# Optimization experiments

Measured on AMD Instinct MI355X. Metric: run time of the kernel, lower is better.

The kernel has to match this reference:

```python
import jax, jax.numpy as jnp
import numpy as np

N_HEAD, DIM, D_K, D_V = 16, 1024, 64, 64
B, L = 4, 2048


def setup_inputs() -> dict:
    key = jax.random.key(0)
    ks = jax.random.split(key, 8)
    def xavier(k, shape, fan_in, fan_out):
        std = float(np.sqrt(2.0 / (fan_in + fan_out)))
        return jax.random.normal(k, shape, dtype=jnp.float32) * std
    return {
        "q": jax.random.normal(ks[0], (B, L, DIM), dtype=jnp.float32),
        "k": jax.random.normal(ks[1], (B, L, DIM), dtype=jnp.float32),
        "v": jax.random.normal(ks[2], (B, L, DIM), dtype=jnp.float32),
        "w_q": xavier(ks[3], (N_HEAD, DIM, D_K), DIM, D_K),
        "w_k": xavier(ks[4], (N_HEAD, DIM, D_K), DIM, D_K),
        "w_v": xavier(ks[5], (N_HEAD, DIM, D_V), DIM, D_V),
        "proj_w": xavier(ks[6], (DIM, N_HEAD * D_V), N_HEAD * D_V, DIM),
        "proj_b": jnp.zeros((DIM,), dtype=jnp.float32),
    }


def reference(q, k, v, w_q, w_k, w_v, proj_w, proj_b):
    batch, len_q, dim = q.shape
    # NOTE: original scales by sqrt(dim) (model dim), not sqrt(d_k)
    scale = jnp.asarray(np.sqrt(dim), dtype=q.dtype)
    # per-head projections: [h, b, q, dk]
    qh = jnp.einsum('bqd,hdk->hbqk', q, w_q)
    kh = jnp.einsum('bsd,hdk->hbsk', k, w_k)
    vh = jnp.einsum('bsd,hdv->hbsv', v, w_v)
    scores = jnp.einsum('hbqk,hbsk->hbqs', qh, kh) / scale
    attn = jax.nn.softmax(scores, axis=-1)
    out = jnp.einsum('hbqs,hbsv->hbqv', attn, vh)
    # concat heads along last dim: [b, q, h*dv] (head-major order, matching torch.cat(split))
    out = jnp.transpose(out, (1, 2, 0, 3)).reshape(batch, len_q, -1)
    # output projection (dropout is identity at eval)
    return out @ proj_w.T + proj_b
```

## Files before the change

kernel.cpp:

```cpp
#include <hip/hip_runtime.h>
#include <hip/hip_bf16.h>
#include <stdint.h>

#define NH 16
#define DM 1024
#define DKV 64
#define BB 4
#define LL 2048
#define MT (BB*LL)
#define NT (LL/64)

typedef __bf16 bf16;
typedef __bf16 bf16x8 __attribute__((ext_vector_type(8)));
typedef float f32x4 __attribute__((ext_vector_type(4)));
typedef float f32x16 __attribute__((ext_vector_type(16)));
typedef unsigned int u32x2 __attribute__((ext_vector_type(2)));
typedef unsigned int u32x4 __attribute__((ext_vector_type(4)));

__device__ __forceinline__ void gload_lds16(const void* g, void* l) {
  __builtin_amdgcn_global_load_lds(
      (const __attribute__((address_space(1))) unsigned int*)g,
      (__attribute__((address_space(3))) unsigned int*)l, 16, 0, 0);
}

__device__ __forceinline__ unsigned short bfbits(float x) {
  bf16 b = (bf16)x;
  return __builtin_bit_cast(unsigned short, b);
}

__device__ __forceinline__ float fast_exp2(float x) {
#if defined(__has_builtin)
#if __has_builtin(__builtin_amdgcn_exp2f)
  return __builtin_amdgcn_exp2f(x);
#else
  float r; asm("v_exp_f32 %0, %1" : "=v"(r) : "v"(x)); return r;
#endif
#else
  float r; asm("v_exp_f32 %0, %1" : "=v"(r) : "v"(x)); return r;
#endif
}

#if defined(__has_builtin)
#if __has_builtin(__builtin_amdgcn_permlane32_swap)
#define HAVE_PLSWAP 1
#endif
#endif

__device__ __forceinline__ u32x2 plswap(unsigned int a, unsigned int b, int hi) {
#ifdef HAVE_PLSWAP
  auto rr = __builtin_amdgcn_permlane32_swap(a, b, false, false);
  u32x2 r; r.x = rr[0]; r.y = rr[1];
  return r;
#else
  unsigned int pa = (unsigned int)__shfl_xor((int)a, 32);
  unsigned int pb_ = (unsigned int)__shfl_xor((int)b, 32);
  u32x2 r;
  r.x = hi ? pb_ : a;
  r.y = hi ? b : pa;
  return r;
#endif
}

__global__ __launch_bounds__(256) void cast3_f32_to_bf16(const float* __restrict__ i0,
                                                         const float* __restrict__ i1,
                                                         const float* __restrict__ i2,
                                                         bf16* __restrict__ o0,
                                                         bf16* __restrict__ o1,
                                                         bf16* __restrict__ o2, int n8) {
  const float* in = blockIdx.y == 0 ? i0 : (blockIdx.y == 1 ? i1 : i2);
  bf16* out = blockIdx.y == 0 ? o0 : (blockIdx.y == 1 ? o1 : o2);
  int i = blockIdx.x * blockDim.x + threadIdx.x;
  if (i >= n8) return;
  const float4* p = (const float4*)in + (size_t)i * 2;
  float4 a = p[0], b = p[1];
  bf16x8 r;
  r[0] = (bf16)a.x; r[1] = (bf16)a.y; r[2] = (bf16)a.z; r[3] = (bf16)a.w;
  r[4] = (bf16)b.x; r[5] = (bf16)b.y; r[6] = (bf16)b.z; r[7] = (bf16)b.w;
  *((bf16x8*)out + i) = r;
}

__global__ __launch_bounds__(256) void cast_f32_to_bf16(const float* __restrict__ in,
                                                        bf16* __restrict__ out, int n8) {
  int i = blockIdx.x * blockDim.x + threadIdx.x;
  if (i >= n8) return;
  const float4* p = (const float4*)in + (size_t)i * 2;
  float4 a = p[0], b = p[1];
  bf16x8 r;
  r[0] = (bf16)a.x; r[1] = (bf16)a.y; r[2] = (bf16)a.z; r[3] = (bf16)a.w;
  r[4] = (bf16)b.x; r[5] = (bf16)b.y; r[6] = (bf16)b.z; r[7] = (bf16)b.w;
  *((bf16x8*)out + i) = r;
}

__global__ __launch_bounds__(256) void repack_w(const float* __restrict__ w0, const float* __restrict__ w1,
                                                const float* __restrict__ w2,
                                                bf16* __restrict__ o0, bf16* __restrict__ o1,
                                                bf16* __restrict__ o2) {
  const float* w = blockIdx.z == 0 ? w0 : (blockIdx.z == 1 ? w1 : w2);
  bf16* o = blockIdx.z == 0 ? o0 : (blockIdx.z == 1 ? o1 : o2);
  __shared__ float t[64][65];
  int h = blockIdx.y, d0 = blockIdx.x * 64;
  const float* src = w + ((size_t)h * DM + d0) * DKV;
  for (int i = threadIdx.x; i < 64 * 64; i += 256) {
    int r = i >> 6, c = i & 63;
    t[r][c] = src[(size_t)r * DKV + c];
  }
  __syncthreads();
  for (int i = threadIdx.x; i < 64 * 64; i += 256) {
    int kk = i >> 6, d = i & 63;
    o[((size_t)(h * 64 + kk)) * DM + d0 + d] = (bf16)t[d][kk];
  }
}

__global__ __launch_bounds__(256) void gemm_qkv(const bf16* __restrict__ Xq, const bf16* __restrict__ Xk,
                                                const bf16* __restrict__ Xv, const bf16* __restrict__ Wqt,
                                                const bf16* __restrict__ Wkt, const bf16* __restrict__ Wvt,
                                                bf16* __restrict__ QH, bf16* __restrict__ KH,
                                                bf16* __restrict__ VT) {
  __shared__ bf16 sA[128 * 64];
  __shared__ bf16 sB[128 * 64];
  const int mode = blockIdx.z;
  const bf16* A  = mode == 0 ? Xq : (mode == 1 ? Xk : Xv);
  const bf16* Bt = mode == 0 ? Wqt : (mode == 1 ? Wkt : Wvt);
  const int tid = threadIdx.x;
  const int w = tid >> 6, l = tid & 63;
  const int c = l & 15, g4 = l >> 4;
  const int wm = w >> 1, wn = w & 1;
  const int m0 = blockIdx.y * 128, n0 = blockIdx.x * 128;

  f32x4 acc[4][4] = {};
  for (int kt = 0; kt < 1024; kt += 64) {
#pragma unroll
    for (int i = 0; i < 4; ++i) {
      int blk = i * 4 + w;
      int row = blk * 8 + (l >> 3);
      int g = (l & 7) ^ (row & 7);
      gload_lds16(A + ((size_t)(m0 + row)) * 1024 + kt + g * 8, (char*)sA + blk * 1024);
      gload_lds16(Bt + ((size_t)(n0 + row)) * 1024 + kt + g * 8, (char*)sB + blk * 1024);
    }
    __syncthreads();
#pragma unroll
    for (int ks = 0; ks < 2; ++ks) {
      bf16x8 af[4], bfr[4];
#pragma unroll
      for (int x = 0; x < 4; ++x) {
        int ar = wm * 64 + x * 16 + c;
        af[x] = *(const bf16x8*)((const char*)sA + ar * 128 + (((ks * 4 + g4) ^ (ar & 7)) * 16));
        int br = wn * 64 + x * 16 + c;
        bfr[x] = *(const bf16x8*)((const char*)sB + br * 128 + (((ks * 4 + g4) ^ (br & 7)) * 16));
      }
#pragma unroll
      for (int x = 0; x < 4; ++x)
#pragma unroll
        for (int y = 0; y < 4; ++y)
          acc[x][y] = __builtin_amdgcn_mfma_f32_16x16x32_bf16(af[x], bfr[y], acc[x][y], 0, 0, 0);
    }
    __syncthreads();
  }

  const int mm = m0 + wm * 64, nn = n0 + wn * 64;
  if (mode < 2) {
    bf16* O = mode == 0 ? QH : KH;
    const float s = (mode == 0) ? 0.03125f * 1.44269504088896f : 1.0f;
#pragma unroll
    for (int x = 0; x < 4; ++x)
#pragma unroll
      for (int y = 0; y < 4; ++y)
#pragma unroll
        for (int r = 0; r < 4; ++r) {
          int m = mm + x * 16 + g4 * 4 + r;
          int n = nn + y * 16 + c;
          O[(size_t)m * 1024 + n] = (bf16)(acc[x][y][r] * s);
        }
  } else {
    bf16* O = VT;
#pragma unroll
    for (int x = 0; x < 4; ++x)
#pragma unroll
      for (int y = 0; y < 4; ++y) {
        int mb = mm + x * 16 + g4 * 4;
        int n = nn + y * 16 + c;
        int bb2 = mb >> 11, sidx = mb & 2047;
        int hh2 = n >> 6, dv = n & 63;
        unsigned int u0 = bfbits(acc[x][y][0]) | ((unsigned int)bfbits(acc[x][y][1]) << 16);
        unsigned int u1 = bfbits(acc[x][y][2]) | ((unsigned int)bfbits(acc[x][y][3]) << 16);
        *(uint2*)(O + ((size_t)((hh2 * 4 + bb2) * 64 + dv)) * LL + sidx) = make_uint2(u0, u1);
      }
  }
}

__global__ __launch_bounds__(256) void gemm_proj(const bf16* __restrict__ A, const bf16* __restrict__ Bt,
                                                 float* __restrict__ Out, const float* __restrict__ bias) {
  __shared__ bf16 sA[128 * 64];
  __shared__ bf16 sB[128 * 64];
  const int tid = threadIdx.x;
  const int w = tid >> 6, l = tid & 63;
  const int c = l & 15, g4 = l >> 4;
  const int wm = w >> 1, wn = w & 1;
  const int m0 = blockIdx.y * 128, n0 = blockIdx.x * 128;

  f32x4 acc[4][4] = {};
  for (int kt = 0; kt < 1024; kt += 64) {
#pragma unroll
    for (int i = 0; i < 4; ++i) {
      int blk = i * 4 + w;
      int row = blk * 8 + (l >> 3);
      int g = (l & 7) ^ (row & 7);
      gload_lds16(A + ((size_t)(m0 + row)) * 1024 + kt + g * 8, (char*)sA + blk * 1024);
      gload_lds16(Bt + ((size_t)(n0 + row)) * 1024 + kt + g * 8, (char*)sB + blk * 1024);
    }
    __syncthreads();
#pragma unroll
    for (int ks = 0; ks < 2; ++ks) {
      bf16x8 af[4], bfr[4];
#pragma unroll
      for (int x = 0; x < 4; ++x) {
        int ar = wm * 64 + x * 16 + c;
        af[x] = *(const bf16x8*)((const char*)sA + ar * 128 + (((ks * 4 + g4) ^ (ar & 7)) * 16));
        int br = wn * 64 + x * 16 + c;
        bfr[x] = *(const bf16x8*)((const char*)sB + br * 128 + (((ks * 4 + g4) ^ (br & 7)) * 16));
      }
#pragma unroll
      for (int x = 0; x < 4; ++x)
#pragma unroll
        for (int y = 0; y < 4; ++y)
          acc[x][y] = __builtin_amdgcn_mfma_f32_16x16x32_bf16(af[x], bfr[y], acc[x][y], 0, 0, 0);
    }
    __syncthreads();
  }

  const int mm = m0 + wm * 64, nn = n0 + wn * 64;
#pragma unroll
  for (int x = 0; x < 4; ++x)
#pragma unroll
    for (int y = 0; y < 4; ++y)
#pragma unroll
      for (int r = 0; r < 4; ++r) {
        int m = mm + x * 16 + g4 * 4 + r;
        int n = nn + y * 16 + c;
        Out[(size_t)m * 1024 + n] = acc[x][y][r] + bias[n];
      }
}

__global__ __launch_bounds__(256, 2) void attn_kernel(const bf16* __restrict__ qh,
                                                      const bf16* __restrict__ kh,
                                                      const bf16* __restrict__ vt,
                                                      bf16* __restrict__ o) {
  __shared__ bf16 sK[4][64 * 64];
  __shared__ bf16 sV[4][64 * 64];
  const int tid = threadIdx.x, w = tid >> 6, l = tid & 63;
  const int c = l & 31, hi = l >> 5;
  const int bh = blockIdx.x, b = bh & 3, h = bh >> 2;
  const int q0 = blockIdx.y * 256 + w * 64;

  const bf16* qbase = qh + ((size_t)(b * LL)) * DM + h * 64;
  const bf16* kbase = kh + ((size_t)(b * LL)) * DM + h * 64;
  const bf16* vbase = vt + ((size_t)((h * 4 + b) * 64)) * LL;

  bf16x8 qfA[4], qfB[4];
#pragma unroll
  for (int ks = 0; ks < 4; ++ks) {
    qfA[ks] = *(const bf16x8*)(qbase + (size_t)(q0 + c) * DM + ks * 16 + hi * 8);
    qfB[ks] = *(const bf16x8*)(qbase + (size_t)(q0 + 32 + c) * DM + ks * 16 + hi * 8);
  }

  bf16x8 onesf;
#pragma unroll
  for (int i = 0; i < 8; ++i) onesf[i] = (bf16)1.0f;

  f32x16 oA0 = {}, oA1 = {}, oB0 = {}, oB1 = {};
  f32x16 lAa = {}, lBa = {};

  auto STAGE = [&](int bufi, int kv0) {
#pragma unroll
    for (int j = 0; j < 2; ++j) {
      int gi = w * 128 + j * 64 + l;
      int row = gi >> 3;
      int g = (gi & 7) ^ (row & 7);
      gload_lds16(kbase + (size_t)(kv0 + row) * DM + g * 8,
                  (char*)sK[bufi] + (w * 128 + j * 64) * 16);
      gload_lds16(vbase + (size_t)row * LL + kv0 + g * 8,
                  (char*)sV[bufi] + (w * 128 + j * 64) * 16);
    }
  };

  auto EXPPACK = [&](f32x16& st0, f32x16& st1, bf16x8* pb) {
#pragma unroll
    for (int r = 0; r < 16; ++r) st0[r] = fast_exp2(st0[r]);
#pragma unroll
    for (int r = 0; r < 16; ++r) st1[r] = fast_exp2(st1[r]);
#pragma unroll
    for (int t = 0; t < 2; ++t) {
      const f32x16& st = t ? st1 : st0;
      unsigned int u[4][2];
#pragma unroll
      for (int g2 = 0; g2 < 4; ++g2) {
        u[g2][0] = (unsigned int)bfbits(st[4 * g2 + 0]) | ((unsigned int)bfbits(st[4 * g2 + 1]) << 16);
        u[g2][1] = (unsigned int)bfbits(st[4 * g2 + 2]) | ((unsigned int)bfbits(st[4 * g2 + 3]) << 16);
      }
      u32x2 s0 = plswap(u[0][0], u[1][0], hi);
      u32x2 s1 = plswap(u[0][1], u[1][1], hi);
      u32x4 w0; w0.x = s0.x; w0.y = s1.x; w0.z = s0.y; w0.w = s1.y;
      pb[2 * t] = __builtin_bit_cast(bf16x8, w0);
      u32x2 s2 = plswap(u[2][0], u[3][0], hi);
      u32x2 s3 = plswap(u[2][1], u[3][1], hi);
      u32x4 w1; w1.x = s2.x; w1.y = s3.x; w1.z = s2.y; w1.w = s3.y;
      pb[2 * t + 1] = __builtin_bit_cast(bf16x8, w1);
    }
  };

  auto TILE = [&](int bufi) {
    const char* Kb = (const char*)sK[bufi];
    const char* Vb = (const char*)sV[bufi];

    bf16x8 kf[8];
#pragma unroll
    for (int ks = 0; ks < 4; ++ks) {
      int slot = ((ks * 2 + hi) ^ (c & 7)) * 16;
      kf[ks]     = *(const bf16x8*)(Kb + c * 128 + slot);
      kf[4 + ks] = *(const bf16x8*)(Kb + (32 + c) * 128 + slot);
    }
    f32x16 sA0 = {}, sA1 = {}, sB0 = {}, sB1 = {};
    __builtin_amdgcn_s_setprio(1);
#pragma unroll
    for (int ks = 0; ks < 4; ++ks) {
      sA0 = __builtin_amdgcn_mfma_f32_32x32x16_bf16(kf[ks],     qfA[ks], sA0, 0, 0, 0);
      sA1 = __builtin_amdgcn_mfma_f32_32x32x16_bf16(kf[4 + ks], qfA[ks], sA1, 0, 0, 0);
    }
#pragma unroll
    for (int ks = 0; ks < 4; ++ks) {
      sB0 = __builtin_amdgcn_mfma_f32_32x32x16_bf16(kf[ks],     qfB[ks], sB0, 0, 0, 0);
      sB1 = __builtin_amdgcn_mfma_f32_32x32x16_bf16(kf[4 + ks], qfB[ks], sB1, 0, 0, 0);
    }
    __builtin_amdgcn_s_setprio(0);

    bf16x8 pbA[4];
    EXPPACK(sA0, sA1, pbA);

    bf16x8 vf[8];
#pragma unroll
    for (int ks = 0; ks < 4; ++ks) {
      int slot = ((ks * 2 + hi) ^ (c & 7)) * 16;
      vf[ks]     = *(const bf16x8*)(Vb + c * 128 + slot);
      vf[4 + ks] = *(const bf16x8*)(Vb + (32 + c) * 128 + slot);
    }
    __builtin_amdgcn_s_setprio(1);
#pragma unroll
    for (int ks = 0; ks < 4; ++ks) {
      oA0 = __builtin_amdgcn_mfma_f32_32x32x16_bf16(vf[ks],     pbA[ks], oA0, 0, 0, 0);
      oA1 = __builtin_amdgcn_mfma_f32_32x32x16_bf16(vf[4 + ks], pbA[ks], oA1, 0, 0, 0);
      lAa = __builtin_amdgcn_mfma_f32_32x32x16_bf16(onesf,      pbA[ks], lAa, 0, 0, 0);
    }
    __builtin_amdgcn_s_setprio(0);

    bf16x8 pbB[4];
    EXPPACK(sB0, sB1, pbB);
    __builtin_amdgcn_s_setprio(1);
#pragma unroll
    for (int ks = 0; ks < 4; ++ks) {
      oB0 = __builtin_amdgcn_mfma_f32_32x32x16_bf16(vf[ks],     pbB[ks], oB0, 0, 0, 0);
      oB1 = __builtin_amdgcn_mfma_f32_32x32x16_bf16(vf[4 + ks], pbB[ks], oB1, 0, 0, 0);
      lBa = __builtin_amdgcn_mfma_f32_32x32x16_bf16(onesf,      pbB[ks], lBa, 0, 0, 0);
    }
    __builtin_amdgcn_s_setprio(0);
  };

  STAGE(0, 0);
  STAGE(1, 64);

  for (int wd = 0; wd < 16; ++wd) {
    __builtin_amdgcn_s_barrier();
    int t2 = 2 * wd + 2;
    if (t2 < NT) {
      STAGE(t2 & 3, t2 * 64);
      STAGE((t2 + 1) & 3, (t2 + 1) * 64);
      asm volatile("s_waitcnt vmcnt(8)" ::: "memory");
    } else {
      asm volatile("s_waitcnt vmcnt(0)" ::: "memory");
    }
    TILE((2 * wd) & 3);
    TILE((2 * wd + 1) & 3);
  }

  bf16* ob = o + ((size_t)(b * LL)) * DM + h * 64;
  {
    float inv = 1.0f / lAa[0];
#pragma unroll
    for (int dt = 0; dt < 2; ++dt) {
      const f32x16& oc = dt ? oA1 : oA0;
#pragma unroll
      for (int rg = 0; rg < 4; ++rg) {
        int dv0 = dt * 32 + rg * 8 + hi * 4;
        unsigned int u0 = (unsigned int)bfbits(oc[rg * 4 + 0] * inv) |
                          ((unsigned int)bfbits(oc[rg * 4 + 1] * inv) << 16);
        unsigned int u1 = (unsigned int)bfbits(oc[rg * 4 + 2] * inv) |
                          ((unsigned int)bfbits(oc[rg * 4 + 3] * inv) << 16);
        *(uint2*)(ob + (size_t)(q0 + c) * DM + dv0) = make_uint2(u0, u1);
      }
    }
  }
  {
    float inv = 1.0f / lBa[0];
#pragma unroll
    for (int dt = 0; dt < 2; ++dt) {
      const f32x16& oc = dt ? oB1 : oB0;
#pragma unroll
      for (int rg = 0; rg < 4; ++rg) {
        int dv0 = dt * 32 + rg * 8 + hi * 4;
        unsigned int u0 = (unsigned int)bfbits(oc[rg * 4 + 0] * inv) |
                          ((unsigned int)bfbits(oc[rg * 4 + 1] * inv) << 16);
        unsigned int u1 = (unsigned int)bfbits(oc[rg * 4 + 2] * inv) |
                          ((unsigned int)bfbits(oc[rg * 4 + 3] * inv) << 16);
        *(uint2*)(ob + (size_t)(q0 + 32 + c) * DM + dv0) = make_uint2(u0, u1);
      }
    }
  }
}

extern "C" void kernel_launch(void* const* d_in, const int* in_sizes, int n_in,
                              void* d_out, int out_size, void* d_ws, size_t ws_size,
                              hipStream_t stream) {
  const float* q  = (const float*)d_in[0];
  const float* k  = (const float*)d_in[1];
  const float* v  = (const float*)d_in[2];
  const float* wq = (const float*)d_in[3];
  const float* wk = (const float*)d_in[4];
  const float* wv = (const float*)d_in[5];
  const float* pw = (const float*)d_in[6];
  const float* pb = (const float*)d_in[7];
  float* out = (float*)d_out;

  char* ws = (char*)d_ws;
  const size_t SX = (size_t)MT * DM * 2;
  const size_t SW = (size_t)DM * DM * 2;
  bf16* Xq  = (bf16*)(ws);
  bf16* Xk  = (bf16*)(ws + SX);
  bf16* Xv  = (bf16*)(ws + 2 * SX);
  bf16* Wqt = (bf16*)(ws + 3 * SX);
  bf16* Wkt = (bf16*)(ws + 3 * SX + SW);
  bf16* Wvt = (bf16*)(ws + 3 * SX + 2 * SW);
  bf16* Wp  = (bf16*)(ws + 3 * SX + 3 * SW);
  bf16* QH  = (bf16*)(ws + 3 * SX + 4 * SW);
  bf16* KH  = (bf16*)(ws + 4 * SX + 4 * SW);
  bf16* VT  = (bf16*)(ws + 5 * SX + 4 * SW);
  bf16* OO  = Xq;

  const int nx8 = MT * DM / 8;
  cast3_f32_to_bf16<<<dim3(nx8 / 256, 3), 256, 0, stream>>>(q, k, v, Xq, Xk, Xv, nx8);
  const int nw8 = DM * DM / 8;
  cast_f32_to_bf16<<<dim3(nw8 / 256), 256, 0, stream>>>(pw, Wp, nw8);
  repack_w<<<dim3(16, 16, 3), 256, 0, stream>>>(wq, wk, wv, Wqt, Wkt, Wvt);

  gemm_qkv<<<dim3(8, 64, 3), 256, 0, stream>>>(Xq, Xk, Xv, Wqt, Wkt, Wvt, QH, KH, VT);

  attn_kernel<<<dim3(64, 8), 256, 0, stream>>>(QH, KH, VT, OO);

  gemm_proj<<<dim3(8, 64), 256, 0, stream>>>(OO, Wp, out, pb);
}
```

Measured before the change: 219.2 us.

## Rewrite QKV GEMM as 256x256 tile, double-buffered, 8-wave pipelined kernel

Replaces the 128x128 single-buffered QKV projection GEMM with a 256x256 tile kernel using 512 threads and double-buffered LDS. Global-to-LDS loads for the next K tile are issued in halves between MFMA phases, with explicit vmcnt gating, barriers and setprio. The aim is to hide load latency behind compute and raise arithmetic intensity per block. It uses 128 KB of LDS per block, which limits occupancy, and produces fewer blocks (384), which risks wave-quantization imbalance across CUs.

```diff
diff --git a/kernel.cpp b/kernel.cpp
--- a/kernel.cpp
+++ b/kernel.cpp
@@ -16,6 +16,8 @@
 typedef float f32x16 __attribute__((ext_vector_type(16)));
 typedef unsigned int u32x2 __attribute__((ext_vector_type(2)));
 typedef unsigned int u32x4 __attribute__((ext_vector_type(4)));
+
+template <int V> struct ic { static constexpr int v = V; };
 
 __device__ __forceinline__ void gload_lds16(const void* g, void* l) {
   __builtin_amdgcn_global_load_lds(
@@ -111,74 +113,123 @@
   }
 }
 
-__global__ __launch_bounds__(256) void gemm_qkv(const bf16* __restrict__ Xq, const bf16* __restrict__ Xk,
-                                                const bf16* __restrict__ Xv, const bf16* __restrict__ Wqt,
-                                                const bf16* __restrict__ Wkt, const bf16* __restrict__ Wvt,
-                                                bf16* __restrict__ QH, bf16* __restrict__ KH,
-                                                bf16* __restrict__ VT) {
-  __shared__ bf16 sA[128 * 64];
-  __shared__ bf16 sB[128 * 64];
+__global__ __launch_bounds__(512, 2) void gemm_qkv256(const bf16* __restrict__ Xq, const bf16* __restrict__ Xk,
+                                                      const bf16* __restrict__ Xv, const bf16* __restrict__ Wqt,
+                                                      const bf16* __restrict__ Wkt, const bf16* __restrict__ Wvt,
+                                                      bf16* __restrict__ QH, bf16* __restrict__ KH,
+                                                      bf16* __restrict__ VT) {
+  __shared__ bf16 sA[2][256 * 64];
+  __shared__ bf16 sB[2][256 * 64];
   const int mode = blockIdx.z;
-  const bf16* A  = mode == 0 ? Xq : (mode == 1 ? Xk : Xv);
-  const bf16* Bt = mode == 0 ? Wqt : (mode == 1 ? Wkt : Wvt);
+  const bf16* Ap  = mode == 0 ? Xq : (mode == 1 ? Xk : Xv);
+  const bf16* Btp = mode == 0 ? Wqt : (mode == 1 ? Wkt : Wvt);
   const int tid = threadIdx.x;
-  const int w = tid >> 6, l = tid & 63;
-  const int c = l & 15, g4 = l >> 4;
-  const int wm = w >> 1, wn = w & 1;
-  const int m0 = blockIdx.y * 128, n0 = blockIdx.x * 128;
-
-  f32x4 acc[4][4] = {};
-  for (int kt = 0; kt < 1024; kt += 64) {
-#pragma unroll
-    for (int i = 0; i < 4; ++i) {
-      int blk = i * 4 + w;
-      int row = blk * 8 + (l >> 3);
-      int g = (l & 7) ^ (row & 7);
-      gload_lds16(A + ((size_t)(m0 + row)) * 1024 + kt + g * 8, (char*)sA + blk * 1024);
-      gload_lds16(Bt + ((size_t)(n0 + row)) * 1024 + kt + g * 8, (char*)sB + blk * 1024);
-    }
-    __syncthreads();
-#pragma unroll
-    for (int ks = 0; ks < 2; ++ks) {
-      bf16x8 af[4], bfr[4];
-#pragma unroll
-      for (int x = 0; x < 4; ++x) {
-        int ar = wm * 64 + x * 16 + c;
-        af[x] = *(const bf16x8*)((const char*)sA + ar * 128 + (((ks * 4 + g4) ^ (ar & 7)) * 16));
-        int br = wn * 64 + x * 16 + c;
-        bfr[x] = *(const bf16x8*)((const char*)sB + br * 128 + (((ks * 4 + g4) ^ (br & 7)) * 16));
-      }
-#pragma unroll
-      for (int x = 0; x < 4; ++x)
-#pragma unroll
-        for (int y = 0; y < 4; ++y)
-          acc[x][y] = __builtin_amdgcn_mfma_f32_16x16x32_bf16(af[x], bfr[y], acc[x][y], 0, 0, 0);
-    }
-    __syncthreads();
-  }
-
-  const int mm = m0 + wm * 64, nn = n0 + wn * 64;
+  const int wid = tid >> 6, l = tid & 63;
+  const int cc = l & 15, g4 = l >> 4;
+  const int wr = wid >> 2, wc = wid & 3;
+  const int m0 = blockIdx.y * 256, n0 = blockIdx.x * 256;
+
+  f32x4 acc[8][4] = {};
+
+  auto STAGEH = [&](auto SB_, auto SI_, auto SH_, int stile) {
+    constexpr int SBUF = decltype(SB_)::v, SISB = decltype(SI_)::v, SHALF = decltype(SH_)::v;
+    int kk = (stile < 16 ? stile : 15) * 64;
+    const bf16* sp = SISB ? Btp : Ap;
+    int b0 = SISB ? n0 : m0;
+    char* db = (char*)(SISB ? &sB[SBUF][0] : &sA[SBUF][0]);
+#pragma unroll
+    for (int j = 0; j < 2; ++j) {
+      int gb = (j * 8 + wid) * 64;
+      int g = gb + l;
+      int rl = g >> 3, gl = g & 7;
+      int row = SHALF * 128 + rl;
+      int slot = gl ^ (row & 7);
+      gload_lds16(sp + (size_t)(b0 + row) * 1024 + kk + slot * 8,
+                  db + (SHALF * 1024 + gb) * 16);
+    }
+  };
+
+  auto PHASE = [&](auto MH_, auto NH_, auto BUF_, auto SB_, auto SI_, auto SH_,
+                   int stile, auto GATE_) {
+    constexpr int MH = decltype(MH_)::v, NHF = decltype(NH_)::v, BUF = decltype(BUF_)::v;
+    constexpr int GATE = decltype(GATE_)::v;
+    bf16x8 af[4][2], bfv[2][2];
+#pragma unroll
+    for (int x2 = 0; x2 < 4; ++x2) {
+      int ar = (2 * (MH * 4 + x2) + wr) * 16 + cc;
+#pragma unroll
+      for (int ks = 0; ks < 2; ++ks)
+        af[x2][ks] = *(const bf16x8*)((const char*)&sA[BUF][0] + ar * 128 +
+                                      (((ks * 4 + g4) ^ (ar & 7)) * 16));
+    }
+#pragma unroll
+    for (int y2 = 0; y2 < 2; ++y2) {
+      int br = (4 * (NHF * 2 + y2) + wc) * 16 + cc;
+#pragma unroll
+      for (int ks = 0; ks < 2; ++ks)
+        bfv[y2][ks] = *(const bf16x8*)((const char*)&sB[BUF][0] + br * 128 +
+                                       (((ks * 4 + g4) ^ (br & 7)) * 16));
+    }
+    STAGEH(SB_, SI_, SH_, stile);
+    __builtin_amdgcn_s_barrier();
+    asm volatile("s_waitcnt lgkmcnt(0)" ::: "memory");
+    __builtin_amdgcn_sched_barrier(0);
+    __builtin_amdgcn_s_setprio(1);
+#pragma unroll
+    for (int x2 = 0; x2 < 4; ++x2)
+#pragma unroll
+      for (int y2 = 0; y2 < 2; ++y2)
+#pragma unroll
+        for (int ks = 0; ks < 2; ++ks)
+          acc[MH * 4 + x2][NHF * 2 + y2] = __builtin_amdgcn_mfma_f32_16x16x32_bf16(
+              af[x2][ks], bfv[y2][ks], acc[MH * 4 + x2][NHF * 2 + y2], 0, 0, 0);
+    __builtin_amdgcn_s_setprio(0);
+    if constexpr (GATE == 8) asm volatile("s_waitcnt vmcnt(8)" ::: "memory");
+    else if constexpr (GATE == 6) asm volatile("s_waitcnt vmcnt(6)" ::: "memory");
+    else if constexpr (GATE == 4) asm volatile("s_waitcnt vmcnt(4)" ::: "memory");
+    __builtin_amdgcn_s_barrier();
+  };
+
+  STAGEH(ic<0>{}, ic<0>{}, ic<0>{}, 0); STAGEH(ic<0>{}, ic<0>{}, ic<1>{}, 0);
+  STAGEH(ic<0>{}, ic<1>{}, ic<0>{}, 0); STAGEH(ic<0>{}, ic<1>{}, ic<1>{}, 0);
+  STAGEH(ic<1>{}, ic<0>{}, ic<0>{}, 1); STAGEH(ic<1>{}, ic<0>{}, ic<1>{}, 1);
+  STAGEH(ic<1>{}, ic<1>{}, ic<0>{}, 1); STAGEH(ic<1>{}, ic<1>{}, ic<1>{}, 1);
+  asm volatile("s_waitcnt vmcnt(0)" ::: "memory");
+  __builtin_amdgcn_s_barrier();
+
+  for (int i = 0; i < 8; ++i) {
+    int t0 = 2 * i;
+    PHASE(ic<0>{}, ic<0>{}, ic<0>{},  ic<1>{}, ic<0>{}, ic<1>{}, t0 + 1, ic<-1>{});
+    PHASE(ic<0>{}, ic<1>{}, ic<0>{},  ic<1>{}, ic<1>{}, ic<1>{}, t0 + 1, ic<-1>{});
+    PHASE(ic<1>{}, ic<0>{}, ic<0>{},  ic<0>{}, ic<0>{}, ic<0>{}, t0 + 2, ic<-1>{});
+    PHASE(ic<1>{}, ic<1>{}, ic<0>{},  ic<0>{}, ic<1>{}, ic<0>{}, t0 + 2, ic<8>{});
+    PHASE(ic<0>{}, ic<0>{}, ic<1>{},  ic<0>{}, ic<0>{}, ic<1>{}, t0 + 2, ic<6>{});
+    PHASE(ic<0>{}, ic<1>{}, ic<1>{},  ic<0>{}, ic<1>{}, ic<1>{}, t0 + 2, ic<-1>{});
+    PHASE(ic<1>{}, ic<0>{}, ic<1>{},  ic<1>{}, ic<0>{}, ic<0>{}, t0 + 3, ic<-1>{});
+    PHASE(ic<1>{}, ic<1>{}, ic<1>{},  ic<1>{}, ic<1>{}, ic<0>{}, t0 + 3, ic<4>{});
+  }
+
   if (mode < 2) {
     bf16* O = mode == 0 ? QH : KH;
     const float s = (mode == 0) ? 0.03125f * 1.44269504088896f : 1.0f;
 #pragma unroll
-    for (int x = 0; x < 4; ++x)
+    for (int x = 0; x < 8; ++x)
 #pragma unroll
       for (int y = 0; y < 4; ++y)
 #pragma unroll
         for (int r = 0; r < 4; ++r) {
-          int m = mm + x * 16 + g4 * 4 + r;
-          int n = nn + y * 16 + c;
+          int m = m0 + (2 * x + wr) * 16 + g4 * 4 + r;
+          int n = n0 + (4 * y + wc) * 16 + cc;
           O[(size_t)m * 1024 + n] = (bf16)(acc[x][y][r] * s);
         }
   } else {
     bf16* O = VT;
 #pragma unroll
-    for (int x = 0; x < 4; ++x)
+    for (int x = 0; x < 8; ++x)
 #pragma unroll
       for (int y = 0; y < 4; ++y) {
-        int mb = mm + x * 16 + g4 * 4;
-        int n = nn + y * 16 + c;
+        int mb = m0 + (2 * x + wr) * 16 + g4 * 4;
+        int n = n0 + (4 * y + wc) * 16 + cc;
         int bb2 = mb >> 11, sidx = mb & 2047;
         int hh2 = n >> 6, dv = n & 63;
         unsigned int u0 = bfbits(acc[x][y][0]) | ((unsigned int)bfbits(acc[x][y][1]) << 16);
@@ -450,7 +501,7 @@
   cast_f32_to_bf16<<<dim3(nw8 / 256), 256, 0, stream>>>(pw, Wp, nw8);
   repack_w<<<dim3(16, 16, 3), 256, 0, stream>>>(wq, wk, wv, Wqt, Wkt, Wvt);
 
-  gemm_qkv<<<dim3(8, 64, 3), 256, 0, stream>>>(Xq, Xk, Xv, Wqt, Wkt, Wvt, QH, KH, VT);
+  gemm_qkv256<<<dim3(4, 32, 3), 512, 0, stream>>>(Xq, Xk, Xv, Wqt, Wkt, Wvt, QH, KH, VT);
 
   attn_kernel<<<dim3(64, 8), 256, 0, stream>>>(QH, KH, VT, OO);
 
```

Measured after the change: 235.9 us. 1.08x slower.

## Split attention work across 8 waves with 32 queries each

Applied to the files above, without the earlier changes.

The attention block grows from 4 to 8 waves, and each wave now owns 32 query rows instead of 64. Per-wave registers roughly halve (one set of accumulators, K/V fragments loaded just in time), and the launch bounds request 4 blocks per CU for more latency hiding. Each thread stages one 16-byte chunk per K/V tile instead of two, and the waitcnt is adjusted to match. In exchange, each wave reads K/V from LDS for half the queries, doubling LDS read traffic per FLOP and lowering MFMA reuse per fragment load.

```diff
diff --git a/kernel.cpp b/kernel.cpp
--- a/kernel.cpp
+++ b/kernel.cpp
@@ -241,7 +241,7 @@
       }
 }
 
-__global__ __launch_bounds__(256, 2) void attn_kernel(const bf16* __restrict__ qh,
+__global__ __launch_bounds__(512, 4) void attn_kernel(const bf16* __restrict__ qh,
                                                       const bf16* __restrict__ kh,
                                                       const bf16* __restrict__ vt,
                                                       bf16* __restrict__ o) {
@@ -250,37 +250,31 @@
   const int tid = threadIdx.x, w = tid >> 6, l = tid & 63;
   const int c = l & 31, hi = l >> 5;
   const int bh = blockIdx.x, b = bh & 3, h = bh >> 2;
-  const int q0 = blockIdx.y * 256 + w * 64;
+  const int q0 = blockIdx.y * 256 + w * 32;
 
   const bf16* qbase = qh + ((size_t)(b * LL)) * DM + h * 64;
   const bf16* kbase = kh + ((size_t)(b * LL)) * DM + h * 64;
   const bf16* vbase = vt + ((size_t)((h * 4 + b) * 64)) * LL;
 
-  bf16x8 qfA[4], qfB[4];
-#pragma unroll
-  for (int ks = 0; ks < 4; ++ks) {
-    qfA[ks] = *(const bf16x8*)(qbase + (size_t)(q0 + c) * DM + ks * 16 + hi * 8);
-    qfB[ks] = *(const bf16x8*)(qbase + (size_t)(q0 + 32 + c) * DM + ks * 16 + hi * 8);
-  }
+  bf16x8 qf[4];
+#pragma unroll
+  for (int ks = 0; ks < 4; ++ks)
+    qf[ks] = *(const bf16x8*)(qbase + (size_t)(q0 + c) * DM + ks * 16 + hi * 8);
 
   bf16x8 onesf;
 #pragma unroll
   for (int i = 0; i < 8; ++i) onesf[i] = (bf16)1.0f;
 
-  f32x16 oA0 = {}, oA1 = {}, oB0 = {}, oB1 = {};
-  f32x16 lAa = {}, lBa = {};
+  f32x16 o0 = {}, o1 = {};
+  f32x16 la = {};
 
   auto STAGE = [&](int bufi, int kv0) {
-#pragma unroll
-    for (int j = 0; j < 2; ++j) {
-      int gi = w * 128 + j * 64 + l;
-      int row = gi >> 3;
-      int g = (gi & 7) ^ (row & 7);
-      gload_lds16(kbase + (size_t)(kv0 + row) * DM + g * 8,
-                  (char*)sK[bufi] + (w * 128 + j * 64) * 16);
-      gload_lds16(vbase + (size_t)row * LL + kv0 + g * 8,
-                  (char*)sV[bufi] + (w * 128 + j * 64) * 16);
-    }
+    int row = tid >> 3;
+    int g = (tid & 7) ^ (row & 7);
+    gload_lds16(kbase + (size_t)(kv0 + row) * DM + g * 8,
+                (char*)sK[bufi] + w * 1024);
+    gload_lds16(vbase + (size_t)row * LL + kv0 + g * 8,
+                (char*)sV[bufi] + w * 1024);
   };
 
   auto EXPPACK = [&](f32x16& st0, f32x16& st1, bf16x8* pb) {
@@ -312,54 +306,30 @@
     const char* Kb = (const char*)sK[bufi];
     const char* Vb = (const char*)sV[bufi];
 
-    bf16x8 kf[8];
+    f32x16 st0 = {}, st1 = {};
+    __builtin_amdgcn_s_setprio(1);
 #pragma unroll
     for (int ks = 0; ks < 4; ++ks) {
       int slot = ((ks * 2 + hi) ^ (c & 7)) * 16;
-      kf[ks]     = *(const bf16x8*)(Kb + c * 128 + slot);
-      kf[4 + ks] = *(const bf16x8*)(Kb + (32 + c) * 128 + slot);
-    }
-    f32x16 sA0 = {}, sA1 = {}, sB0 = {}, sB1 = {};
+      bf16x8 k0 = *(const bf16x8*)(Kb + c * 128 + slot);
+      bf16x8 k1 = *(const bf16x8*)(Kb + (32 + c) * 128 + slot);
+      st0 = __builtin_amdgcn_mfma_f32_32x32x16_bf16(k0, qf[ks], st0, 0, 0, 0);
+      st1 = __builtin_amdgcn_mfma_f32_32x32x16_bf16(k1, qf[ks], st1, 0, 0, 0);
+    }
+    __builtin_amdgcn_s_setprio(0);
+
+    bf16x8 pb[4];
+    EXPPACK(st0, st1, pb);
+
     __builtin_amdgcn_s_setprio(1);
-#pragma unroll
-    for (int ks = 0; ks < 4; ++ks) {
-      sA0 = __builtin_amdgcn_mfma_f32_32x32x16_bf16(kf[ks],     qfA[ks], sA0, 0, 0, 0);
-      sA1 = __builtin_amdgcn_mfma_f32_32x32x16_bf16(kf[4 + ks], qfA[ks], sA1, 0, 0, 0);
-    }
-#pragma unroll
-    for (int ks = 0; ks < 4; ++ks) {
-      sB0 = __builtin_amdgcn_mfma_f32_32x32x16_bf16(kf[ks],     qfB[ks], sB0, 0, 0, 0);
-      sB1 = __builtin_amdgcn_mfma_f32_32x32x16_bf16(kf[4 + ks], qfB[ks], sB1, 0, 0, 0);
-    }
-    __builtin_amdgcn_s_setprio(0);
-
-    bf16x8 pbA[4];
-    EXPPACK(sA0, sA1, pbA);
-
-    bf16x8 vf[8];
 #pragma unroll
     for (int ks = 0; ks < 4; ++ks) {
       int slot = ((ks * 2 + hi) ^ (c & 7)) * 16;
-      vf[ks]     = *(const bf16x8*)(Vb + c * 128 + slot);
-      vf[4 + ks] = *(const bf16x8*)(Vb + (32 + c) * 128 + slot);
-    }
-    __builtin_amdgcn_s_setprio(1);
-#pragma unroll
-    for (int ks = 0; ks < 4; ++ks) {
-      oA0 = __builtin_amdgcn_mfma_f32_32x32x16_bf16(vf[ks],     pbA[ks], oA0, 0, 0, 0);
-      oA1 = __builtin_amdgcn_mfma_f32_32x32x16_bf16(vf[4 + ks], pbA[ks], oA1, 0, 0, 0);
-      lAa = __builtin_amdgcn_mfma_f32_32x32x16_bf16(onesf,      pbA[ks], lAa, 0, 0, 0);
-    }
-    __builtin_amdgcn_s_setprio(0);
-
-    bf16x8 pbB[4];
-    EXPPACK(sB0, sB1, pbB);
-    __builtin_amdgcn_s_setprio(1);
-#pragma unroll
-    for (int ks = 0; ks < 4; ++ks) {
-      oB0 = __builtin_amdgcn_mfma_f32_32x32x16_bf16(vf[ks],     pbB[ks], oB0, 0, 0, 0);
-      oB1 = __builtin_amdgcn_mfma_f32_32x32x16_bf16(vf[4 + ks], pbB[ks], oB1, 0, 0, 0);
-      lBa = __builtin_amdgcn_mfma_f32_32x32x16_bf16(onesf,      pbB[ks], lBa, 0, 0, 0);
+      bf16x8 v0 = *(const bf16x8*)(Vb + c * 128 + slot);
+      bf16x8 v1 = *(const bf16x8*)(Vb + (32 + c) * 128 + slot);
+      o0 = __builtin_amdgcn_mfma_f32_32x32x16_bf16(v0, pb[ks], o0, 0, 0, 0);
+      o1 = __builtin_amdgcn_mfma_f32_32x32x16_bf16(v1, pb[ks], o1, 0, 0, 0);
+      la = __builtin_amdgcn_mfma_f32_32x32x16_bf16(onesf, pb[ks], la, 0, 0, 0);
     }
     __builtin_amdgcn_s_setprio(0);
   };
@@ -373,7 +343,7 @@
     if (t2 < NT) {
       STAGE(t2 & 3, t2 * 64);
       STAGE((t2 + 1) & 3, (t2 + 1) * 64);
-      asm volatile("s_waitcnt vmcnt(8)" ::: "memory");
+      asm volatile("s_waitcnt vmcnt(4)" ::: "memory");
     } else {
       asm volatile("s_waitcnt vmcnt(0)" ::: "memory");
     }
@@ -382,36 +352,18 @@
   }
 
   bf16* ob = o + ((size_t)(b * LL)) * DM + h * 64;
-  {
-    float inv = 1.0f / lAa[0];
-#pragma unroll
-    for (int dt = 0; dt < 2; ++dt) {
-      const f32x16& oc = dt ? oA1 : oA0;
-#pragma unroll
-      for (int rg = 0; rg < 4; ++rg) {
-        int dv0 = dt * 32 + rg * 8 + hi * 4;
-        unsigned int u0 = (unsigned int)bfbits(oc[rg * 4 + 0] * inv) |
-                          ((unsigned int)bfbits(oc[rg * 4 + 1] * inv) << 16);
-        unsigned int u1 = (unsigned int)bfbits(oc[rg * 4 + 2] * inv) |
-                          ((unsigned int)bfbits(oc[rg * 4 + 3] * inv) << 16);
-        *(uint2*)(ob + (size_t)(q0 + c) * DM + dv0) = make_uint2(u0, u1);
-      }
-    }
-  }
-  {
-    float inv = 1.0f / lBa[0];
-#pragma unroll
-    for (int dt = 0; dt < 2; ++dt) {
-      const f32x16& oc = dt ? oB1 : oB0;
-#pragma unroll
-      for (int rg = 0; rg < 4; ++rg) {
-        int dv0 = dt * 32 + rg * 8 + hi * 4;
-        unsigned int u0 = (unsigned int)bfbits(oc[rg * 4 + 0] * inv) |
-                          ((unsigned int)bfbits(oc[rg * 4 + 1] * inv) << 16);
-        unsigned int u1 = (unsigned int)bfbits(oc[rg * 4 + 2] * inv) |
-                          ((unsigned int)bfbits(oc[rg * 4 + 3] * inv) << 16);
-        *(uint2*)(ob + (size_t)(q0 + 32 + c) * DM + dv0) = make_uint2(u0, u1);
-      }
+  float inv = 1.0f / la[0];
+#pragma unroll
+  for (int dt = 0; dt < 2; ++dt) {
+    const f32x16& oc = dt ? o1 : o0;
+#pragma unroll
+    for (int rg = 0; rg < 4; ++rg) {
+      int dv0 = dt * 32 + rg * 8 + hi * 4;
+      unsigned int u0 = (unsigned int)bfbits(oc[rg * 4 + 0] * inv) |
+                        ((unsigned int)bfbits(oc[rg * 4 + 1] * inv) << 16);
+      unsigned int u1 = (unsigned int)bfbits(oc[rg * 4 + 2] * inv) |
+                        ((unsigned int)bfbits(oc[rg * 4 + 3] * inv) << 16);
+      *(uint2*)(ob + (size_t)(q0 + c) * DM + dv0) = make_uint2(u0, u1);
     }
   }
 }
@@ -452,7 +404,7 @@
 
   gemm_qkv<<<dim3(8, 64, 3), 256, 0, stream>>>(Xq, Xk, Xv, Wqt, Wkt, Wvt, QH, KH, VT);
 
-  attn_kernel<<<dim3(64, 8), 256, 0, stream>>>(QH, KH, VT, OO);
+  attn_kernel<<<dim3(64, 8), 512, 0, stream>>>(QH, KH, VT, OO);
 
   gemm_proj<<<dim3(8, 64), 256, 0, stream>>>(OO, Wp, out, pb);
 }
```

Measured after the change: 230.6 us. 5.2% more time.

## Fuse fp32-to-bf16 activation cast into QKV GEMM and merge weight prep kernels

Applied to the files above, without the earlier changes.

The separate pass that casts the q/k/v activations to bf16 is removed. The QKV GEMM now streams fp32 tiles straight into LDS with a swizzled layout and packs them to bf16 in registers just before the MFMA. The proj-weight cast is also folded into the weight repack kernel, which cuts the launch count. This avoids writing and rereading bf16 copies of the activations, at the cost of twice the LDS footprint and global traffic for the A operand inside the GEMM, since each A tile is reloaded across the 8 N-blocks.

```diff
diff --git a/kernel.cpp b/kernel.cpp
--- a/kernel.cpp
+++ b/kernel.cpp
@@ -61,65 +61,58 @@
 #endif
 }
 
-__global__ __launch_bounds__(256) void cast3_f32_to_bf16(const float* __restrict__ i0,
-                                                         const float* __restrict__ i1,
-                                                         const float* __restrict__ i2,
-                                                         bf16* __restrict__ o0,
-                                                         bf16* __restrict__ o1,
-                                                         bf16* __restrict__ o2, int n8) {
-  const float* in = blockIdx.y == 0 ? i0 : (blockIdx.y == 1 ? i1 : i2);
-  bf16* out = blockIdx.y == 0 ? o0 : (blockIdx.y == 1 ? o1 : o2);
-  int i = blockIdx.x * blockDim.x + threadIdx.x;
-  if (i >= n8) return;
-  const float4* p = (const float4*)in + (size_t)i * 2;
-  float4 a = p[0], b = p[1];
-  bf16x8 r;
-  r[0] = (bf16)a.x; r[1] = (bf16)a.y; r[2] = (bf16)a.z; r[3] = (bf16)a.w;
-  r[4] = (bf16)b.x; r[5] = (bf16)b.y; r[6] = (bf16)b.z; r[7] = (bf16)b.w;
-  *((bf16x8*)out + i) = r;
-}
-
-__global__ __launch_bounds__(256) void cast_f32_to_bf16(const float* __restrict__ in,
-                                                        bf16* __restrict__ out, int n8) {
-  int i = blockIdx.x * blockDim.x + threadIdx.x;
-  if (i >= n8) return;
-  const float4* p = (const float4*)in + (size_t)i * 2;
-  float4 a = p[0], b = p[1];
-  bf16x8 r;
-  r[0] = (bf16)a.x; r[1] = (bf16)a.y; r[2] = (bf16)a.z; r[3] = (bf16)a.w;
-  r[4] = (bf16)b.x; r[5] = (bf16)b.y; r[6] = (bf16)b.z; r[7] = (bf16)b.w;
-  *((bf16x8*)out + i) = r;
-}
-
-__global__ __launch_bounds__(256) void repack_w(const float* __restrict__ w0, const float* __restrict__ w1,
-                                                const float* __restrict__ w2,
-                                                bf16* __restrict__ o0, bf16* __restrict__ o1,
-                                                bf16* __restrict__ o2) {
-  const float* w = blockIdx.z == 0 ? w0 : (blockIdx.z == 1 ? w1 : w2);
-  bf16* o = blockIdx.z == 0 ? o0 : (blockIdx.z == 1 ? o1 : o2);
+__device__ __forceinline__ bf16x8 pack8(const f32x4& lo, const f32x4& hi2) {
+  u32x4 u;
+  u.x = (unsigned int)bfbits(lo[0]) | ((unsigned int)bfbits(lo[1]) << 16);
+  u.y = (unsigned int)bfbits(lo[2]) | ((unsigned int)bfbits(lo[3]) << 16);
+  u.z = (unsigned int)bfbits(hi2[0]) | ((unsigned int)bfbits(hi2[1]) << 16);
+  u.w = (unsigned int)bfbits(hi2[2]) | ((unsigned int)bfbits(hi2[3]) << 16);
+  return __builtin_bit_cast(bf16x8, u);
+}
+
+__global__ __launch_bounds__(256) void prep_w(const float* __restrict__ w0, const float* __restrict__ w1,
+                                              const float* __restrict__ w2, const float* __restrict__ pw,
+                                              bf16* __restrict__ o0, bf16* __restrict__ o1,
+                                              bf16* __restrict__ o2, bf16* __restrict__ Wp) {
   __shared__ float t[64][65];
-  int h = blockIdx.y, d0 = blockIdx.x * 64;
-  const float* src = w + ((size_t)h * DM + d0) * DKV;
-  for (int i = threadIdx.x; i < 64 * 64; i += 256) {
-    int r = i >> 6, c = i & 63;
-    t[r][c] = src[(size_t)r * DKV + c];
-  }
-  __syncthreads();
-  for (int i = threadIdx.x; i < 64 * 64; i += 256) {
-    int kk = i >> 6, d = i & 63;
-    o[((size_t)(h * 64 + kk)) * DM + d0 + d] = (bf16)t[d][kk];
-  }
-}
-
-__global__ __launch_bounds__(256) void gemm_qkv(const bf16* __restrict__ Xq, const bf16* __restrict__ Xk,
-                                                const bf16* __restrict__ Xv, const bf16* __restrict__ Wqt,
+  if (blockIdx.z < 3) {
+    const float* w = blockIdx.z == 0 ? w0 : (blockIdx.z == 1 ? w1 : w2);
+    bf16* o = blockIdx.z == 0 ? o0 : (blockIdx.z == 1 ? o1 : o2);
+    int h = blockIdx.y, d0 = blockIdx.x * 64;
+    const float* src = w + ((size_t)h * DM + d0) * DKV;
+    for (int i = threadIdx.x; i < 64 * 64; i += 256) {
+      int r = i >> 6, c = i & 63;
+      t[r][c] = src[(size_t)r * DKV + c];
+    }
+    __syncthreads();
+    for (int i = threadIdx.x; i < 64 * 64; i += 256) {
+      int kk = i >> 6, d = i & 63;
+      o[((size_t)(h * 64 + kk)) * DM + d0 + d] = (bf16)t[d][kk];
+    }
+  } else {
+    int base = ((blockIdx.y * 16 + blockIdx.x) * 256 + threadIdx.x) * 2;
+#pragma unroll
+    for (int e = 0; e < 2; ++e) {
+      int i = base + e;
+      const float4* p = (const float4*)pw + (size_t)i * 2;
+      float4 a = p[0], b = p[1];
+      bf16x8 r;
+      r[0] = (bf16)a.x; r[1] = (bf16)a.y; r[2] = (bf16)a.z; r[3] = (bf16)a.w;
+      r[4] = (bf16)b.x; r[5] = (bf16)b.y; r[6] = (bf16)b.z; r[7] = (bf16)b.w;
+      *((bf16x8*)Wp + i) = r;
+    }
+  }
+}
+
+__global__ __launch_bounds__(256) void gemm_qkv(const float* __restrict__ Qf, const float* __restrict__ Kf,
+                                                const float* __restrict__ Vf, const bf16* __restrict__ Wqt,
                                                 const bf16* __restrict__ Wkt, const bf16* __restrict__ Wvt,
                                                 bf16* __restrict__ QH, bf16* __restrict__ KH,
                                                 bf16* __restrict__ VT) {
-  __shared__ bf16 sA[128 * 64];
+  __shared__ float sAf[128 * 64];
   __shared__ bf16 sB[128 * 64];
   const int mode = blockIdx.z;
-  const bf16* A  = mode == 0 ? Xq : (mode == 1 ? Xk : Xv);
+  const float* A = mode == 0 ? Qf : (mode == 1 ? Kf : Vf);
   const bf16* Bt = mode == 0 ? Wqt : (mode == 1 ? Wkt : Wvt);
   const int tid = threadIdx.x;
   const int w = tid >> 6, l = tid & 63;
@@ -130,11 +123,18 @@
   f32x4 acc[4][4] = {};
   for (int kt = 0; kt < 1024; kt += 64) {
 #pragma unroll
+    for (int j = 0; j < 8; ++j) {
+      int gi = j * 256 + tid;
+      int row = gi >> 4, slot = gi & 15;
+      int sg = slot ^ (row & 15);
+      gload_lds16(A + (size_t)(m0 + row) * 1024 + kt + sg * 4,
+                  (char*)sAf + (j * 256 + w * 64) * 16);
+    }
+#pragma unroll
     for (int i = 0; i < 4; ++i) {
       int blk = i * 4 + w;
       int row = blk * 8 + (l >> 3);
       int g = (l & 7) ^ (row & 7);
-      gload_lds16(A + ((size_t)(m0 + row)) * 1024 + kt + g * 8, (char*)sA + blk * 1024);
       gload_lds16(Bt + ((size_t)(n0 + row)) * 1024 + kt + g * 8, (char*)sB + blk * 1024);
     }
     __syncthreads();
@@ -144,7 +144,11 @@
 #pragma unroll
       for (int x = 0; x < 4; ++x) {
         int ar = wm * 64 + x * 16 + c;
-        af[x] = *(const bf16x8*)((const char*)sA + ar * 128 + (((ks * 4 + g4) ^ (ar & 7)) * 16));
+        int p0 = ks * 8 + g4 * 2;
+        int s0 = p0 ^ (ar & 15), s1 = (p0 + 1) ^ (ar & 15);
+        f32x4 lo = *(const f32x4*)((const char*)sAf + ar * 256 + s0 * 16);
+        f32x4 hi2 = *(const f32x4*)((const char*)sAf + ar * 256 + s1 * 16);
+        af[x] = pack8(lo, hi2);
         int br = wn * 64 + x * 16 + c;
         bfr[x] = *(const bf16x8*)((const char*)sB + br * 128 + (((ks * 4 + g4) ^ (br & 7)) * 16));
       }
@@ -432,25 +436,18 @@
   char* ws = (char*)d_ws;
   const size_t SX = (size_t)MT * DM * 2;
   const size_t SW = (size_t)DM * DM * 2;
-  bf16* Xq  = (bf16*)(ws);
-  bf16* Xk  = (bf16*)(ws + SX);
-  bf16* Xv  = (bf16*)(ws + 2 * SX);
-  bf16* Wqt = (bf16*)(ws + 3 * SX);
-  bf16* Wkt = (bf16*)(ws + 3 * SX + SW);
-  bf16* Wvt = (bf16*)(ws + 3 * SX + 2 * SW);
-  bf16* Wp  = (bf16*)(ws + 3 * SX + 3 * SW);
-  bf16* QH  = (bf16*)(ws + 3 * SX + 4 * SW);
-  bf16* KH  = (bf16*)(ws + 4 * SX + 4 * SW);
-  bf16* VT  = (bf16*)(ws + 5 * SX + 4 * SW);
-  bf16* OO  = Xq;
-
-  const int nx8 = MT * DM / 8;
-  cast3_f32_to_bf16<<<dim3(nx8 / 256, 3), 256, 0, stream>>>(q, k, v, Xq, Xk, Xv, nx8);
-  const int nw8 = DM * DM / 8;
-  cast_f32_to_bf16<<<dim3(nw8 / 256), 256, 0, stream>>>(pw, Wp, nw8);
-  repack_w<<<dim3(16, 16, 3), 256, 0, stream>>>(wq, wk, wv, Wqt, Wkt, Wvt);
-
-  gemm_qkv<<<dim3(8, 64, 3), 256, 0, stream>>>(Xq, Xk, Xv, Wqt, Wkt, Wvt, QH, KH, VT);
+  bf16* Wqt = (bf16*)(ws);
+  bf16* Wkt = (bf16*)(ws + SW);
+  bf16* Wvt = (bf16*)(ws + 2 * SW);
+  bf16* Wp  = (bf16*)(ws + 3 * SW);
+  bf16* QH  = (bf16*)(ws + 4 * SW);
+  bf16* KH  = (bf16*)(ws + 4 * SW + SX);
+  bf16* VT  = (bf16*)(ws + 4 * SW + 2 * SX);
+  bf16* OO  = (bf16*)(ws + 4 * SW + 3 * SX);
+
+  prep_w<<<dim3(16, 16, 4), 256, 0, stream>>>(wq, wk, wv, pw, Wqt, Wkt, Wvt, Wp);
+
+  gemm_qkv<<<dim3(8, 64, 3), 256, 0, stream>>>(q, k, v, Wqt, Wkt, Wvt, QH, KH, VT);
 
   attn_kernel<<<dim3(64, 8), 256, 0, stream>>>(QH, KH, VT, OO);
 
```

New measurement: 243.7 us. +11.2%, slower.
